# Optimization experiments

Hardware: AMD Instinct MI355X
Metric: run time of the kernel (lower is better)

The kernel has to match this reference:

```python
import jax, jax.numpy as jnp
import numpy as np

N = 2048          # num nodes
C = 256           # dense_dim per input
EMB = 3 * C       # 768
H = 8             # num_heads
D = EMB // H      # 96 head_dim
ALPHA = 0.2       # leaky relu slope
SCALE = D ** -0.5


def setup_inputs() -> dict:
    key = jax.random.key(0)
    ks = jax.random.split(key, 9)
    sd = EMB ** -0.5
    return {
        "eh": jax.random.normal(ks[0], (N, C), jnp.float32),
        "er": jax.random.normal(ks[1], (N, C), jnp.float32),
        "et": jax.random.normal(ks[2], (N, C), jnp.float32),
        "h_id": jax.random.randint(ks[3], (N,), 0, 32),
        "W_w": jax.random.normal(ks[4], (EMB, EMB), jnp.float32) * sd,
        "a": jax.random.normal(ks[5], (2 * D, 1), jnp.float32) * (2 * D) ** -0.5,
        "proj_w": jax.random.normal(ks[6], (EMB, EMB), jnp.float32) * sd,
        "proj_b": jnp.zeros((EMB,), jnp.float32),
        "skip_w": jax.random.normal(ks[7], (EMB, EMB), jnp.float32) * sd,
        "skip_b": jnp.zeros((EMB,), jnp.float32),
    }


def reference(eh, er, et, h_id, W_w, a, proj_w, proj_b, skip_w, skip_b):
    n = eh.shape[0]
    e = jnp.concatenate([eh, er, et], axis=-1)            # [N, EMB]
    Wh = (e @ W_w.T).reshape(n, H, D)                     # [N, H, D]

    # score = leakyrelu(a1 . Wh_scrambled[i] + a2 . Wh[j]) * scale
    a1, a2 = a[:D, 0], a[D:, 0]
    s1 = Wh @ a1                                          # [N, H]
    s2 = Wh @ a2                                          # [N, H]
    # torch's Wh.repeat(1,1,N).view(N*N,H,D) reads head (j*H + h)//N for pair (i,j,h)
    qidx = (jnp.arange(n)[:, None] * H + jnp.arange(H)[None, :]) // n  # [N, H]
    x = s1[:, qidx] + s2[None, :, :]                      # [N, N, H]
    e_ij = jnp.where(x >= 0, x, ALPHA * x) * SCALE

    mask = h_id[:, None] != h_id[None, :]                 # [N, N]
    e_ij = jnp.where(mask[:, :, None], -jnp.inf, e_ij)
    attn = jax.nn.softmax(e_ij, axis=1)                   # softmax over neighbors j

    out = jnp.einsum('ijh,jhd->ihd', attn, Wh).reshape(n, H * D)
    out = out @ proj_w.T + proj_b                         # [N, EMB]
    skip = e @ skip_w.T + skip_b                          # [N, EMB]
    return skip + out
```

## Files before the change

### kernel.cpp

```cpp
#include <hip/hip_runtime.h>
#include <hip/hip_bf16.h>

#define N_NODES 2048
#define EMB 768
#define NH 8
#define DH 96
#define ALPHA 0.2f
#define SCALE 0.10206207261596575f
#define NGMAX 192
#define WSZ (EMB * EMB)

typedef __bf16 bf16x8 __attribute__((ext_vector_type(8)));
typedef float f32x4 __attribute__((ext_vector_type(4)));
typedef __attribute__((address_space(3))) unsigned int lds_u32;
typedef __attribute__((address_space(1))) const unsigned int glb_u32;

union pack4 { ushort4 u; __hip_bfloat16 h[4]; };

__global__ __launch_bounds__(256) void prep_kernel(
    const float* __restrict__ eh, const float* __restrict__ er, const float* __restrict__ et,
    const float* __restrict__ W0, const float* __restrict__ W1, const float* __restrict__ W2,
    __hip_bfloat16* __restrict__ e, __hip_bfloat16* __restrict__ o0,
    __hip_bfloat16* __restrict__ o1, __hip_bfloat16* __restrict__ o2, int* __restrict__ cnt)
{
    const int b = blockIdx.x;
    const int gtid = b * 256 + threadIdx.x;
    if (gtid < 32) cnt[gtid] = 0;
    const float* src;
    __hip_bfloat16* dst;
    if (b < 1536) {
        int idx = gtid * 4;
        int i = idx / EMB, c = idx % EMB;
        if (c < 256)      src = eh + i * 256 + c;
        else if (c < 512) src = er + i * 256 + (c - 256);
        else              src = et + i * 256 + (c - 512);
        dst = e + (size_t)i * EMB + c;
    } else {
        int idx = (gtid - 1536 * 256) * 4;
        if (idx < WSZ)          { src = W0 + idx;           dst = o0 + idx; }
        else if (idx < 2 * WSZ) { src = W1 + idx - WSZ;     dst = o1 + idx - WSZ; }
        else                    { src = W2 + idx - 2 * WSZ; dst = o2 + idx - 2 * WSZ; }
    }
    float4 v = *reinterpret_cast<const float4*>(src);
    pack4 p;
    p.h[0] = __float2bfloat16(v.x);
    p.h[1] = __float2bfloat16(v.y);
    p.h[2] = __float2bfloat16(v.z);
    p.h[3] = __float2bfloat16(v.w);
    *reinterpret_cast<ushort4*>(dst) = p.u;
}

__device__ __forceinline__ void stage128(
    const __hip_bfloat16* __restrict__ src, int row0, int k0,
    __hip_bfloat16* lds, int wave, int lane)
{
#pragma unroll
    for (int i = 0; i < 4; i++) {
        const int c0 = wave * 256 + i * 64;
        const int c = c0 + lane;
        const int row = c >> 4;
        const int cb = (c & 15) ^ (row & 15);
        const __hip_bfloat16* g = src + (size_t)(row0 + row) * EMB + k0 + cb * 8;
        __builtin_amdgcn_global_load_lds((glb_u32*)g, (lds_u32*)(lds + c0 * 8), 16, 0, 0);
    }
}

__global__ __launch_bounds__(256) void gemm_kernel(
    const __hip_bfloat16* __restrict__ A,
    const __hip_bfloat16* __restrict__ B1, const __hip_bfloat16* __restrict__ B2,
    const float* __restrict__ bias1, const float* __restrict__ bias2,
    float* __restrict__ C1, float* __restrict__ C2,
    int nbn1, int accum)
{
    __shared__ __attribute__((aligned(16))) __hip_bfloat16 sm[2][2][8192];

    const int t = threadIdx.x;
    const int lane = t & 63, wave = t >> 6;
    const int wm = wave >> 1, wn = wave & 1;
    const int bnb = blockIdx.x;
    const bool second = bnb >= nbn1;
    const __hip_bfloat16* B = second ? B2 : B1;
    float* Cf = second ? C2 : C1;
    const int bn = (second ? bnb - nbn1 : bnb) * 64;
    const int bm = blockIdx.y * 64;
    const int l15 = lane & 15, quad = lane >> 4;
    const int rA = wm * 32 + l15, rB = wn * 32 + l15;

    f32x4 acc00 = {0.f,0.f,0.f,0.f}, acc01 = {0.f,0.f,0.f,0.f};
    f32x4 acc10 = {0.f,0.f,0.f,0.f}, acc11 = {0.f,0.f,0.f,0.f};

    stage128(A, bm, 0, &sm[0][0][0], wave, lane);
    stage128(B, bn, 0, &sm[0][1][0], wave, lane);

#pragma unroll 1
    for (int s = 0; s < 6; s++) {
        __syncthreads();
        if (s + 1 < 6) {
            const int k0 = (s + 1) * 128;
            stage128(A, bm, k0, &sm[(s + 1) & 1][0][0], wave, lane);
            stage128(B, bn, k0, &sm[(s + 1) & 1][1][0], wave, lane);
        }
        const __hip_bfloat16* At = &sm[s & 1][0][0];
        const __hip_bfloat16* Bt = &sm[s & 1][1][0];
#pragma unroll
        for (int ks = 0; ks < 4; ks++) {
            const int cq = ks * 4 + quad;
            bf16x8 a0 = *(const bf16x8*)(At + (size_t)(rA * 16        + (cq ^ l15)) * 8);
            bf16x8 a1 = *(const bf16x8*)(At + (size_t)((rA + 16) * 16 + (cq ^ l15)) * 8);
            bf16x8 b0 = *(const bf16x8*)(Bt + (size_t)(rB * 16        + (cq ^ l15)) * 8);
            bf16x8 b1 = *(const bf16x8*)(Bt + (size_t)((rB + 16) * 16 + (cq ^ l15)) * 8);
            acc00 = __builtin_amdgcn_mfma_f32_16x16x32_bf16(a0, b0, acc00, 0, 0, 0);
            acc01 = __builtin_amdgcn_mfma_f32_16x16x32_bf16(a0, b1, acc01, 0, 0, 0);
            acc10 = __builtin_amdgcn_mfma_f32_16x16x32_bf16(a1, b0, acc10, 0, 0, 0);
            acc11 = __builtin_amdgcn_mfma_f32_16x16x32_bf16(a1, b1, acc11, 0, 0, 0);
        }
    }

    const int col0 = bn + wn * 32 + l15;
    const int col1 = col0 + 16;
    float bv0 = 0.f, bv1 = 0.f;
    if (second && bias1 != nullptr) {
        bv0 = bias1[col0] + bias2[col0];
        bv1 = bias1[col1] + bias2[col1];
    }
    const int r0 = bm + wm * 32 + quad * 4;
#pragma unroll
    for (int r = 0; r < 4; r++) {
        const int row0 = r0 + r, row1 = r0 + 16 + r;
        float* p00 = &Cf[(size_t)row0 * EMB + col0];
        float* p01 = &Cf[(size_t)row0 * EMB + col1];
        float* p10 = &Cf[(size_t)row1 * EMB + col0];
        float* p11 = &Cf[(size_t)row1 * EMB + col1];
        if (accum) {
            *p00 += acc00[r];
            *p01 += acc01[r];
            *p10 += acc10[r];
            *p11 += acc11[r];
        } else {
            *p00 = acc00[r] + bv0;
            *p01 = acc01[r] + bv1;
            *p10 = acc10[r] + bv0;
            *p11 = acc11[r] + bv1;
        }
    }
}

__global__ __launch_bounds__(256) void s12g_kernel(
    const float* __restrict__ Wh, const float* __restrict__ a,
    float* __restrict__ s1, float* __restrict__ s2,
    const int* __restrict__ h_id, int* __restrict__ cnt, int* __restrict__ lists)
{
    int gid = blockIdx.x * 256 + threadIdx.x;
    if (gid < N_NODES) {
        int g = h_id[gid];
        int p = atomicAdd(&cnt[g], 1);
        lists[g * N_NODES + p] = gid;
    }
    int i = gid >> 3, h = gid & 7;
    const float* wr = Wh + (size_t)i * EMB + h * DH;
    float acc1 = 0.f, acc2 = 0.f;
    for (int d = 0; d < DH; d++) {
        float w = wr[d];
        acc1 += w * a[d];
        acc2 += w * a[DH + d];
    }
    s1[gid] = acc1;
    s2[gid] = acc2;
}

__global__ __launch_bounds__(256) void attn_kernel(
    const float* __restrict__ Wh, const float* __restrict__ s1, const float* __restrict__ s2,
    const int* __restrict__ cnt, const int* __restrict__ lists,
    __hip_bfloat16* __restrict__ out)
{
    const int g  = blockIdx.x & 31;
    const int h  = (blockIdx.x >> 5) & 7;
    const int dh = blockIdx.x >> 8;
    const int t  = threadIdx.x;

    __shared__ int   jb[NGMAX];
    __shared__ int   qg[NGMAX];
    __shared__ float s2g[NGMAX];
    __shared__ float s1g[NGMAX][9];
    __shared__ float Whg[NGMAX][48];

    const int ng = min(cnt[g], NGMAX);
    const int* gl = lists + g * N_NODES;

    for (int j = t; j < ng; j += 256) {
        int node = gl[j];
        jb[j]  = node;
        qg[j]  = node >> 8;
        s2g[j] = s2[node * 8 + h];
        float4 v0 = *reinterpret_cast<const float4*>(s1 + node * 8);
        float4 v1 = *reinterpret_cast<const float4*>(s1 + node * 8 + 4);
        s1g[j][0] = v0.x; s1g[j][1] = v0.y; s1g[j][2] = v0.z; s1g[j][3] = v0.w;
        s1g[j][4] = v1.x; s1g[j][5] = v1.y; s1g[j][6] = v1.z; s1g[j][7] = v1.w;
    }
    __syncthreads();
    for (int idx = t; idx < ng * 12; idx += 256) {
        int jc = idx / 12, dq = idx % 12;
        float4 v = *reinterpret_cast<const float4*>(
            Wh + (size_t)jb[jc] * EMB + h * DH + dh * 48 + dq * 4);
        *reinterpret_cast<float4*>(&Whg[jc][dq * 4]) = v;
    }
    __syncthreads();

    const int half = t >> 7;
    const int d0 = half * 24;
    for (int tr = t & 127; tr < ng; tr += 128) {
        float m = -1e30f;
        for (int j = 0; j < ng; j++) {
            float x = s1g[tr][qg[j]] + s2g[j];
            float ev = (x >= 0.f ? x : ALPHA * x) * SCALE;
            m = fmaxf(m, ev);
        }
        float S = 0.f;
        for (int j = 0; j < ng; j++) {
            float x = s1g[tr][qg[j]] + s2g[j];
            float ev = (x >= 0.f ? x : ALPHA * x) * SCALE;
            S += __expf(ev - m);
        }
        const float ri = 1.f / S;

        float acc[24];
#pragma unroll
        for (int d = 0; d < 24; d++) acc[d] = 0.f;
        for (int j = 0; j < ng; j++) {
            float x = s1g[tr][qg[j]] + s2g[j];
            float ev = (x >= 0.f ? x : ALPHA * x) * SCALE;
            float p = __expf(ev - m) * ri;
#pragma unroll
            for (int d = 0; d < 24; d++) acc[d] += p * Whg[j][d0 + d];
        }
        __hip_bfloat16* po = out + (size_t)jb[tr] * EMB + h * DH + dh * 48 + d0;
#pragma unroll
        for (int d = 0; d < 24; d += 4) {
            pack4 pk;
            pk.h[0] = __float2bfloat16(acc[d]);
            pk.h[1] = __float2bfloat16(acc[d + 1]);
            pk.h[2] = __float2bfloat16(acc[d + 2]);
            pk.h[3] = __float2bfloat16(acc[d + 3]);
            *reinterpret_cast<ushort4*>(po + d) = pk.u;
        }
    }
}

extern "C" void kernel_launch(void* const* d_in, const int* in_sizes, int n_in,
                              void* d_out, int out_size, void* d_ws, size_t ws_size,
                              hipStream_t stream)
{
    const float* eh     = (const float*)d_in[0];
    const float* er     = (const float*)d_in[1];
    const float* et     = (const float*)d_in[2];
    const int*   h_id   = (const int*)d_in[3];
    const float* W_w    = (const float*)d_in[4];
    const float* a      = (const float*)d_in[5];
    const float* proj_w = (const float*)d_in[6];
    const float* proj_b = (const float*)d_in[7];
    const float* skip_w = (const float*)d_in[8];
    const float* skip_b = (const float*)d_in[9];
    float* out = (float*)d_out;

    char* ws = (char*)d_ws;
    __hip_bfloat16* e_ws   = (__hip_bfloat16*)(ws);
    float*          Wh_ws  = (float*)(ws + 3145728);
    __hip_bfloat16* at_ws  = (__hip_bfloat16*)(ws + 9437184);
    __hip_bfloat16* Wb_ws  = (__hip_bfloat16*)(ws + 12582912);
    __hip_bfloat16* Pb_ws  = (__hip_bfloat16*)(ws + 13762560);
    __hip_bfloat16* Sb_ws  = (__hip_bfloat16*)(ws + 14942208);
    float*          s1_ws  = (float*)(ws + 16121856);
    float*          s2_ws  = (float*)(ws + 16187392);
    int*            cnt_ws = (int*)(ws + 16252928);
    int*            lst_ws = (int*)(ws + 16253056);

    prep_kernel<<<3264, 256, 0, stream>>>(eh, er, et, W_w, proj_w, skip_w,
                                          e_ws, Wb_ws, Pb_ws, Sb_ws, cnt_ws);

    gemm_kernel<<<dim3(24, 32), 256, 0, stream>>>(
        e_ws, Wb_ws, Sb_ws, proj_b, skip_b, Wh_ws, out, 12, 0);

    s12g_kernel<<<64, 256, 0, stream>>>(Wh_ws, a, s1_ws, s2_ws, h_id, cnt_ws, lst_ws);

    attn_kernel<<<512, 256, 0, stream>>>(Wh_ws, s1_ws, s2_ws, cnt_ws, lst_ws, at_ws);

    gemm_kernel<<<dim3(12, 32), 256, 0, stream>>>(
        at_ws, Pb_ws, nullptr, nullptr, nullptr, out, nullptr, 12, 1);
}
```

Before: 134.2 us.

## Enlarge GEMM M-tile to 128 and use triple-buffered 64-wide K pipeline

```diff
diff --git a/kernel.cpp b/kernel.cpp
--- a/kernel.cpp
+++ b/kernel.cpp
@@ -50,7 +50,7 @@
     *reinterpret_cast<ushort4*>(dst) = p.u;
 }
 
-__device__ __forceinline__ void stage128(
+__device__ __forceinline__ void stageA64(
     const __hip_bfloat16* __restrict__ src, int row0, int k0,
     __hip_bfloat16* lds, int wave, int lane)
 {
@@ -58,8 +58,22 @@
     for (int i = 0; i < 4; i++) {
         const int c0 = wave * 256 + i * 64;
         const int c = c0 + lane;
-        const int row = c >> 4;
-        const int cb = (c & 15) ^ (row & 15);
+        const int row = c >> 3;
+        const int cb = (c & 7) ^ (row & 7);
+        const __hip_bfloat16* g = src + (size_t)(row0 + row) * EMB + k0 + cb * 8;
+        __builtin_amdgcn_global_load_lds((glb_u32*)g, (lds_u32*)(lds + c0 * 8), 16, 0, 0);
+    }
+}
+__device__ __forceinline__ void stageB64(
+    const __hip_bfloat16* __restrict__ src, int row0, int k0,
+    __hip_bfloat16* lds, int wave, int lane)
+{
+#pragma unroll
+    for (int i = 0; i < 2; i++) {
+        const int c0 = wave * 128 + i * 64;
+        const int c = c0 + lane;
+        const int row = c >> 3;
+        const int cb = (c & 7) ^ (row & 7);
         const __hip_bfloat16* g = src + (size_t)(row0 + row) * EMB + k0 + cb * 8;
         __builtin_amdgcn_global_load_lds((glb_u32*)g, (lds_u32*)(lds + c0 * 8), 16, 0, 0);
     }
@@ -72,7 +86,8 @@
     float* __restrict__ C1, float* __restrict__ C2,
     int nbn1, int accum)
 {
-    __shared__ __attribute__((aligned(16))) __hip_bfloat16 sm[2][2][8192];
+    __shared__ __attribute__((aligned(16))) __hip_bfloat16 smA[3][8192];
+    __shared__ __attribute__((aligned(16))) __hip_bfloat16 smB[3][4096];
 
     const int t = threadIdx.x;
     const int lane = t & 63, wave = t >> 6;
@@ -82,38 +97,57 @@
     const __hip_bfloat16* B = second ? B2 : B1;
     float* Cf = second ? C2 : C1;
     const int bn = (second ? bnb - nbn1 : bnb) * 64;
-    const int bm = blockIdx.y * 64;
+    const int bm = blockIdx.y * 128;
     const int l15 = lane & 15, quad = lane >> 4;
-    const int rA = wm * 32 + l15, rB = wn * 32 + l15;
-
-    f32x4 acc00 = {0.f,0.f,0.f,0.f}, acc01 = {0.f,0.f,0.f,0.f};
-    f32x4 acc10 = {0.f,0.f,0.f,0.f}, acc11 = {0.f,0.f,0.f,0.f};
-
-    stage128(A, bm, 0, &sm[0][0][0], wave, lane);
-    stage128(B, bn, 0, &sm[0][1][0], wave, lane);
-
+
+    f32x4 acc00 = {0,0,0,0}, acc01 = {0,0,0,0};
+    f32x4 acc10 = {0,0,0,0}, acc11 = {0,0,0,0};
+    f32x4 acc20 = {0,0,0,0}, acc21 = {0,0,0,0};
+    f32x4 acc30 = {0,0,0,0}, acc31 = {0,0,0,0};
+
+    const int ra0 = wm * 64 + l15;
+    const int rb0 = wn * 32 + l15;
+    const int xa = ra0 & 7;
+    const int xb = rb0 & 7;
+
+    stageA64(A, bm, 0, &smA[0][0], wave, lane);
+    stageB64(B, bn, 0, &smB[0][0], wave, lane);
+
+    int bufc = 0;
 #pragma unroll 1
-    for (int s = 0; s < 6; s++) {
-        __syncthreads();
-        if (s + 1 < 6) {
-            const int k0 = (s + 1) * 128;
-            stage128(A, bm, k0, &sm[(s + 1) & 1][0][0], wave, lane);
-            stage128(B, bn, k0, &sm[(s + 1) & 1][1][0], wave, lane);
-        }
-        const __hip_bfloat16* At = &sm[s & 1][0][0];
-        const __hip_bfloat16* Bt = &sm[s & 1][1][0];
-#pragma unroll
-        for (int ks = 0; ks < 4; ks++) {
+    for (int s = 0; s < 12; s++) {
+        const int bufn = (bufc == 2) ? 0 : bufc + 1;
+        if (s + 1 < 12) {
+            const int k0 = (s + 1) * 64;
+            stageA64(A, bm, k0, &smA[bufn][0], wave, lane);
+            stageB64(B, bn, k0, &smB[bufn][0], wave, lane);
+            asm volatile("s_waitcnt vmcnt(6)" ::: "memory");
+        } else {
+            asm volatile("s_waitcnt vmcnt(0)" ::: "memory");
+        }
+        __builtin_amdgcn_s_barrier();
+
+        const __hip_bfloat16* At = &smA[bufc][0];
+        const __hip_bfloat16* Bt = &smB[bufc][0];
+#pragma unroll
+        for (int ks = 0; ks < 2; ks++) {
             const int cq = ks * 4 + quad;
-            bf16x8 a0 = *(const bf16x8*)(At + (size_t)(rA * 16        + (cq ^ l15)) * 8);
-            bf16x8 a1 = *(const bf16x8*)(At + (size_t)((rA + 16) * 16 + (cq ^ l15)) * 8);
-            bf16x8 b0 = *(const bf16x8*)(Bt + (size_t)(rB * 16        + (cq ^ l15)) * 8);
-            bf16x8 b1 = *(const bf16x8*)(Bt + (size_t)((rB + 16) * 16 + (cq ^ l15)) * 8);
+            bf16x8 a0 = *(const bf16x8*)(At + (size_t)((ra0     ) * 8 + (cq ^ xa)) * 8);
+            bf16x8 a1 = *(const bf16x8*)(At + (size_t)((ra0 + 16) * 8 + (cq ^ xa)) * 8);
+            bf16x8 a2 = *(const bf16x8*)(At + (size_t)((ra0 + 32) * 8 + (cq ^ xa)) * 8);
+            bf16x8 a3 = *(const bf16x8*)(At + (size_t)((ra0 + 48) * 8 + (cq ^ xa)) * 8);
+            bf16x8 b0 = *(const bf16x8*)(Bt + (size_t)((rb0     ) * 8 + (cq ^ xb)) * 8);
+            bf16x8 b1 = *(const bf16x8*)(Bt + (size_t)((rb0 + 16) * 8 + (cq ^ xb)) * 8);
             acc00 = __builtin_amdgcn_mfma_f32_16x16x32_bf16(a0, b0, acc00, 0, 0, 0);
             acc01 = __builtin_amdgcn_mfma_f32_16x16x32_bf16(a0, b1, acc01, 0, 0, 0);
             acc10 = __builtin_amdgcn_mfma_f32_16x16x32_bf16(a1, b0, acc10, 0, 0, 0);
             acc11 = __builtin_amdgcn_mfma_f32_16x16x32_bf16(a1, b1, acc11, 0, 0, 0);
-        }
+            acc20 = __builtin_amdgcn_mfma_f32_16x16x32_bf16(a2, b0, acc20, 0, 0, 0);
+            acc21 = __builtin_amdgcn_mfma_f32_16x16x32_bf16(a2, b1, acc21, 0, 0, 0);
+            acc30 = __builtin_amdgcn_mfma_f32_16x16x32_bf16(a3, b0, acc30, 0, 0, 0);
+            acc31 = __builtin_amdgcn_mfma_f32_16x16x32_bf16(a3, b1, acc31, 0, 0, 0);
+        }
+        bufc = bufn;
     }
 
     const int col0 = bn + wn * 32 + l15;
@@ -123,24 +157,24 @@
         bv0 = bias1[col0] + bias2[col0];
         bv1 = bias1[col1] + bias2[col1];
     }
-    const int r0 = bm + wm * 32 + quad * 4;
+    const int r0 = bm + wm * 64 + quad * 4;
 #pragma unroll
     for (int r = 0; r < 4; r++) {
-        const int row0 = r0 + r, row1 = r0 + 16 + r;
-        float* p00 = &Cf[(size_t)row0 * EMB + col0];
-        float* p01 = &Cf[(size_t)row0 * EMB + col1];
-        float* p10 = &Cf[(size_t)row1 * EMB + col0];
-        float* p11 = &Cf[(size_t)row1 * EMB + col1];
+        const int rw0 = r0 + r, rw1 = rw0 + 16, rw2 = rw0 + 32, rw3 = rw0 + 48;
+        float* p00 = &Cf[(size_t)rw0 * EMB + col0]; float* p01 = &Cf[(size_t)rw0 * EMB + col1];
+        float* p10 = &Cf[(size_t)rw1 * EMB + col0]; float* p11 = &Cf[(size_t)rw1 * EMB + col1];
+        float* p20 = &Cf[(size_t)rw2 * EMB + col0]; float* p21 = &Cf[(size_t)rw2 * EMB + col1];
+        float* p30 = &Cf[(size_t)rw3 * EMB + col0]; float* p31 = &Cf[(size_t)rw3 * EMB + col1];
         if (accum) {
-            *p00 += acc00[r];
-            *p01 += acc01[r];
-            *p10 += acc10[r];
-            *p11 += acc11[r];
+            *p00 += acc00[r]; *p01 += acc01[r];
+            *p10 += acc10[r]; *p11 += acc11[r];
+            *p20 += acc20[r]; *p21 += acc21[r];
+            *p30 += acc30[r]; *p31 += acc31[r];
         } else {
-            *p00 = acc00[r] + bv0;
-            *p01 = acc01[r] + bv1;
-            *p10 = acc10[r] + bv0;
-            *p11 = acc11[r] + bv1;
+            *p00 = acc00[r] + bv0; *p01 = acc01[r] + bv1;
+            *p10 = acc10[r] + bv0; *p11 = acc11[r] + bv1;
+            *p20 = acc20[r] + bv0; *p21 = acc21[r] + bv1;
+            *p30 = acc30[r] + bv0; *p31 = acc31[r] + bv1;
         }
     }
 }
@@ -277,13 +311,13 @@
     prep_kernel<<<3264, 256, 0, stream>>>(eh, er, et, W_w, proj_w, skip_w,
                                           e_ws, Wb_ws, Pb_ws, Sb_ws, cnt_ws);
 
-    gemm_kernel<<<dim3(24, 32), 256, 0, stream>>>(
+    gemm_kernel<<<dim3(24, 16), 256, 0, stream>>>(
         e_ws, Wb_ws, Sb_ws, proj_b, skip_b, Wh_ws, out, 12, 0);
 
     s12g_kernel<<<64, 256, 0, stream>>>(Wh_ws, a, s1_ws, s2_ws, h_id, cnt_ws, lst_ws);
 
     attn_kernel<<<512, 256, 0, stream>>>(Wh_ws, s1_ws, s2_ws, cnt_ws, lst_ws, at_ws);
 
-    gemm_kernel<<<dim3(12, 32), 256, 0, stream>>>(
+    gemm_kernel<<<dim3(12, 16), 256, 0, stream>>>(
         at_ws, Pb_ws, nullptr, nullptr, nullptr, out, nullptr, 12, 1);
 }
```

Result: slower. 137.3 us (+2.3%).
